# Performance work log

Hardware: AMD Instinct MI355X
Metric: run time of the kernel (lower is better)

## Reference

```python
import jax, jax.numpy as jnp
import numpy as np

H = 256  # hidden_size
I = 18   # input_size
B = 1024 # batch
T = 1024 # seq_len


def setup_inputs() -> dict:
    key = jax.random.key(0)
    ks = jax.random.split(key, 8)
    scale = 1.0 / np.sqrt(H)  # matches torch GRUCell uniform init scale roughly
    s = lambda k, shape: jax.random.normal(k, shape, dtype=jnp.float32) * scale
    return {
        "x": jax.random.normal(ks[0], (B, T, I), dtype=jnp.float32),
        # layer 0 GRUCell params (gate order r, z, n as in torch)
        "W_ih0": s(ks[1], (3 * H, I)),
        "W_hh0": s(ks[2], (3 * H, H)),
        "b_ih0": jnp.zeros((3 * H,), dtype=jnp.float32),
        "b_hh0": jnp.zeros((3 * H,), dtype=jnp.float32),
        # layer 1 GRUCell params
        "W_ih1": s(ks[3], (3 * H, H)),
        "W_hh1": s(ks[4], (3 * H, H)),
        "b_ih1": jnp.zeros((3 * H,), dtype=jnp.float32),
        "b_hh1": jnp.zeros((3 * H,), dtype=jnp.float32),
        "fc_w": s(ks[5], (1, H)),
        "fc_b": jnp.zeros((1,), dtype=jnp.float32),
    }


def _gru_cell(x, h, W_ih, W_hh, b_ih, b_hh):
    # torch.nn.GRUCell math, gate order (r, z, n)
    gi = x @ W_ih.T + b_ih  # (B, 3H)
    gh = h @ W_hh.T + b_hh  # (B, 3H)
    ir, iz, inn = jnp.split(gi, 3, axis=-1)
    hr, hz, hn = jnp.split(gh, 3, axis=-1)
    r = jax.nn.sigmoid(ir + hr)
    z = jax.nn.sigmoid(iz + hz)
    n = jnp.tanh(inn + r * hn)
    return (1.0 - z) * n + z * h


def reference(x, W_ih0, W_hh0, b_ih0, b_hh0, W_ih1, W_hh1, b_ih1, b_hh1, fc_w, fc_b):
    batch = x.shape[0]
    hid = W_hh0.shape[1]
    h_init = (jnp.zeros((batch, hid), dtype=x.dtype),
              jnp.zeros((batch, hid), dtype=x.dtype))
    xs = jnp.swapaxes(x, 0, 1)  # (T, B, I) for scan over time

    def step(carry, xt):
        h0, h1 = carry
        h0 = _gru_cell(xt, h0, W_ih0, W_hh0, b_ih0, b_hh0)
        h1 = _gru_cell(h0, h1, W_ih1, W_hh1, b_ih1, b_hh1)
        return (h0, h1), None

    (h0, h1), _ = jax.lax.scan(step, h_init, xs)
    return h1 @ fc_w.T + fc_b  # (B, 1)
```

## Files before the change

kernel.cpp:

```cpp
#include <hip/hip_runtime.h>

#define B_ 1024
#define T_ 1024
#define I_ 18
#define H_ 256
#define NCHUNK 16
#define NSLICE 16

typedef _Float16 f16;
typedef _Float16 f16x8 __attribute__((ext_vector_type(8)));
typedef float f32x4 __attribute__((ext_vector_type(4)));

#define MFMA16(a, b, c) __builtin_amdgcn_mfma_f32_16x16x32_f16((a), (b), (c), 0, 0, 0)
#define SB() __builtin_amdgcn_sched_barrier(0)

#define WF_FRAGS 75
#define WF_SLICE (WF_FRAGS * 512)
#define WF_TOTAL (NSLICE * WF_SLICE)
#define HB0 WF_TOTAL
#define HB_TOTAL (2 * 2 * NCHUNK * 8 * 4 * 512)
#define PART_B ((HB0 + HB_TOTAL) * 2)
#define FLAG_B (PART_B + 1024 * 16 * 4)
#define NFLAGS (NCHUNK * 4 * 32)
#define IDS_B (FLAG_B + NFLAGS * 4)
#define DEC_B (IDS_B + 256 * 4)
#define F_IH0(g) (g)
#define F_HH0(g, kt) (3 + (g) * 8 + (kt))
#define F_IH1(g, kt) (27 + (g) * 8 + (kt))
#define F_HH1(g, kt) (51 + (g) * 8 + (kt))

struct TrueT { static constexpr bool value = true; };
struct FalseT { static constexpr bool value = false; };

__device__ __forceinline__ int hfrag(int layer, int par, int chunk, int kt, int m) {
  return ((((layer * 2 + par) * NCHUNK + chunk) * 8 + kt) * 4 + m) * 512;
}

__global__ void init_ws(f16* __restrict__ ws) {
  int i = blockIdx.x * blockDim.x + threadIdx.x;
  unsigned* hb = (unsigned*)(ws + HB0);
  for (int k = i; k < HB_TOTAL / 2; k += gridDim.x * blockDim.x) hb[k] = 0u;
  int* flg = (int*)((char*)ws + FLAG_B);
  if (i < NFLAGS + 256 + 1) flg[i] = 0;
}

__global__ void prep_weights(const float* __restrict__ Wih0,
                             const float* __restrict__ Whh0,
                             const float* __restrict__ Wih1,
                             const float* __restrict__ Whh1,
                             f16* __restrict__ ws) {
  int tid = blockIdx.x * blockDim.x + threadIdx.x;
  if (tid >= NSLICE * WF_FRAGS * 64) return;
  int lane = tid & 63;
  int f = (tid >> 6) % WF_FRAGS;
  int s = tid / (WF_FRAGS * 64);
  int lrow = lane & 15, lgrp = lane >> 4;
  f16 v[8];
  if (f < 3) {
    int n = f * H_ + s * 16 + lrow;
#pragma unroll
    for (int j = 0; j < 8; ++j) {
      int k = lgrp * 8 + j;
      v[j] = (k < I_) ? (f16)Wih0[n * I_ + k] : (f16)0.f;
    }
  } else {
    int ff;
    const float* W;
    if (f < 27) { ff = f - 3;  W = Whh0; }
    else if (f < 51) { ff = f - 27; W = Wih1; }
    else { ff = f - 51; W = Whh1; }
    int g = ff >> 3, kt = ff & 7;
    int n = g * H_ + s * 16 + lrow;
    int kb = kt * 32 + lgrp * 8;
#pragma unroll
    for (int j = 0; j < 8; ++j) v[j] = (f16)W[n * H_ + kb + j];
  }
  *(f16x8*)(ws + ((size_t)s * WF_SLICE + f * 512 + lane * 8)) = *(f16x8*)v;
}

__device__ __forceinline__ float sigm(float v) {
  v = fminf(fmaxf(v, -30.f), 30.f);
  return __builtin_amdgcn_rcpf(1.f + __expf(-v));
}
__device__ __forceinline__ float tanh_fast(float v) {
  v = fminf(fmaxf(v, -15.f), 15.f);
  float e = __expf(-2.f * v);
  return (1.f - e) * __builtin_amdgcn_rcpf(1.f + e);
}

template <bool FAST>
__device__ __forceinline__ f16x8 ldh(const f16* p) {
  f16x8 r;
  if (FAST)
    asm volatile("global_load_dwordx4 %0, %1, off nt" : "=&v"(r) : "v"(p));
  else
    asm volatile("global_load_dwordx4 %0, %1, off sc0 sc1" : "=&v"(r) : "v"(p));
  return r;
}
template <bool FAST>
__device__ __forceinline__ void sth(f16* p, f16 v) {
  unsigned u = (unsigned)__builtin_bit_cast(unsigned short, v);
  if (FAST)
    asm volatile("global_store_short %0, %1, off" ::"v"(p), "v"(u) : "memory");
  else
    asm volatile("global_store_short %0, %1, off sc0 sc1" ::"v"(p), "v"(u)
                 : "memory");
}
template <bool FAST>
__device__ __forceinline__ void stf(int* p, int v) {
  if (FAST)
    asm volatile("global_store_dword %0, %1, off" ::"v"(p), "v"(v) : "memory");
  else
    asm volatile("global_store_dword %0, %1, off sc0 sc1" ::"v"(p), "v"(v)
                 : "memory");
}
__device__ __forceinline__ int ld_sys(const int* p) {
  int r;
  asm volatile("global_load_dword %0, %1, off sc0 sc1\n\ts_waitcnt vmcnt(0)"
               : "=&v"(r) : "v"(p) : "memory");
  return r;
}
__device__ __forceinline__ void st_sys(int* p, int v) { stf<false>(p, v); }
__device__ __forceinline__ f32x4 ldx4(const float* p) {
  f32x4 r;
  asm volatile("global_load_dwordx4 %0, %1, off" : "=&v"(r) : "v"(p));
  return r;
}

__global__ __launch_bounds__(256, 1) void gru_main(
    const float* __restrict__ x, const float* __restrict__ bih0,
    const float* __restrict__ bhh0, const float* __restrict__ bih1,
    const float* __restrict__ bhh1, const float* __restrict__ fcw,
    f16* __restrict__ ws) {
  const int tid = threadIdx.x;
  const int wv = tid >> 6, lane = tid & 63;
  const int lrow = lane & 15, lgrp = lane >> 4;
  const int chunk = blockIdx.x & 15, slice = blockIdx.x >> 4;

  f16x8 wf[WF_FRAGS];
  {
    const f16* wb = ws + (size_t)slice * WF_SLICE + lane * 8;
#pragma unroll
    for (int f = 0; f < WF_FRAGS; ++f) wf[f] = *(const f16x8*)(wb + f * 512);
  }

  const int c = slice * 16 + lrow;
  const float bR0 = bih0[c] + bhh0[c], bZ0 = bih0[H_ + c] + bhh0[H_ + c];
  const float bI0 = bih0[2 * H_ + c], bH0 = bhh0[2 * H_ + c];
  const float bR1 = bih1[c] + bhh1[c], bZ1 = bih1[H_ + c] + bhh1[H_ + c];
  const float bI1 = bih1[2 * H_ + c], bH1 = bhh1[2 * H_ + c];
  const float fw = fcw[c];

  float h0r[4] = {0.f, 0.f, 0.f, 0.f}, h1r[4] = {0.f, 0.f, 0.f, 0.f};

  f16* hb = ws + HB0;
  int* flags = (int*)((char*)ws + FLAG_B);
  const int* fpoll = flags + (chunk * 4 + wv) * 32 + (lane & 31);
  int* fpost0 = flags + (chunk * 4 + wv) * 32 + slice;
  int* fpost1 = fpost0 + 16;
  int* ids = (int*)((char*)ws + IDS_B);
  int* dec = (int*)((char*)ws + DEC_B);
  const int rbase = chunk * 64 + wv * 16;
  const float* xrow = x + (size_t)(rbase + lrow) * T_ * I_;
  const int s_kt = slice >> 1;
  const int s_off = 128 * ((slice & 1) * 2 + (lrow >> 3)) + (lrow & 7);
  const int o1 = (lgrp == 0) ? 0 : (lgrp == 1) ? 8 : (lgrp == 2) ? 14 : 0;
  const int o2 = (lgrp == 0) ? 4 : (lgrp == 1) ? 12 : 0;
  int dead = 0;

  {
    unsigned xcc;
    asm volatile("s_getreg_b32 %0, hwreg(HW_REG_XCC_ID)" : "=s"(xcc));
    if (tid == 0) st_sys(ids + blockIdx.x, (int)xcc + 1);
    if (blockIdx.x == 0 && wv == 0) {
      int ok, guard = 0;
      for (;;) {
        int v0 = ld_sys(ids + lane * 4 + 0), v1 = ld_sys(ids + lane * 4 + 1);
        int v2 = ld_sys(ids + lane * 4 + 2), v3 = ld_sys(ids + lane * 4 + 3);
        ok = (v0 && v1 && v2 && v3);
        if (__all(ok)) { ok = 1; break; }
        if (++guard > (1 << 16)) { ok = 0; break; }
        __builtin_amdgcn_s_sleep(8);
      }
      int verdict = 1;
      if (ok) {
        int eq = 1;
        if (lane < 16) {
          int r0 = ld_sys(ids + lane);
          for (int s = 1; s < 16; ++s)
            eq &= (ld_sys(ids + s * 16 + lane) == r0);
        }
        verdict = __all(eq) ? 2 : 1;
      }
      if (lane == 0) st_sys(dec, verdict);
    }
  }
  int decision = 1;
  {
    int g = 0;
    for (;;) {
      int d = ld_sys(dec);
      if (d) { decision = d; break; }
      if (++g > (1 << 20)) break;
      __builtin_amdgcn_s_sleep(8);
    }
  }

  auto phase_loop = [&](auto FC) {
    constexpr bool F = decltype(FC)::value;
    asm volatile("s_waitcnt vmcnt(0)" ::: "memory");
    SB();
    f32x4 xA1 = ldx4(xrow + o1);
    f32x4 xA2 = ldx4(xrow + o2);

    for (int p = 0; p <= T_; ++p) {
      if (p > 0 && !dead) {
        int tgt = (lane & 16) ? p - 1 : p;
        int guard = 0;
        for (;;) {
          int v;
          if (F)
            asm volatile("global_load_dword %0, %1, off nt"
                         : "=&v"(v) : "v"(fpoll));
          else
            asm volatile("global_load_dword %0, %1, off sc0 sc1"
                         : "=&v"(v) : "v"(fpoll));
          asm volatile("s_waitcnt vmcnt(0)" ::: "memory");
          if (__all(v >= tgt)) break;
          if (++guard > (1 << 18)) { dead = 1; break; }
          __builtin_amdgcn_s_sleep(1);
        }
      }
      SB();
      f16x8 ah0[8], ah1[8];
      {
        const f16* b0 = hb + hfrag(0, (p + 1) & 1, chunk, 0, wv) + lane * 8;
        const f16* b1 = hb + hfrag(1, p & 1, chunk, 0, wv) + lane * 8;
#pragma unroll
        for (int kt = 0; kt < 8; ++kt) ah0[kt] = ldh<F>(b0 + kt * 2048);
#pragma unroll
        for (int kt = 0; kt < 8; ++kt) ah1[kt] = ldh<F>(b1 + kt * 2048);
      }
      SB();
      asm volatile("s_waitcnt vmcnt(12)" ::: "memory");
      SB();
      f16x8 ax;
      {
        float s0 = (lgrp == 2) ? xA1[2] : xA1[0];
        float s1 = (lgrp == 2) ? xA1[3] : xA1[1];
        ax[0] = (f16)s0;     ax[1] = (f16)s1;
        ax[2] = (f16)xA1[2]; ax[3] = (f16)xA1[3];
        ax[4] = (f16)xA2[0]; ax[5] = (f16)xA2[1];
        ax[6] = (f16)xA2[2]; ax[7] = (f16)xA2[3];
      }
      f32x4 aR0 = {bR0, bR0, bR0, bR0}, aZ0 = {bZ0, bZ0, bZ0, bZ0};
      f32x4 aI0 = {bI0, bI0, bI0, bI0}, aH0 = {bH0, bH0, bH0, bH0};
      f32x4 aR1 = {bR1, bR1, bR1, bR1}, aZ1 = {bZ1, bZ1, bZ1, bZ1};
      f32x4 aI1 = {bI1, bI1, bI1, bI1}, aH1 = {bH1, bH1, bH1, bH1};
#pragma unroll
      for (int kt = 0; kt < 4; ++kt) {
        aR0 = MFMA16(ah0[kt], wf[F_HH0(0, kt)], aR0);
        aZ0 = MFMA16(ah0[kt], wf[F_HH0(1, kt)], aZ0);
        aH0 = MFMA16(ah0[kt], wf[F_HH0(2, kt)], aH0);
      }
      SB();
      asm volatile("s_waitcnt vmcnt(8)" ::: "memory");
      SB();
      aR0 = MFMA16(ax, wf[F_IH0(0)], aR0);
      aZ0 = MFMA16(ax, wf[F_IH0(1)], aZ0);
      aI0 = MFMA16(ax, wf[F_IH0(2)], aI0);
#pragma unroll
      for (int kt = 4; kt < 8; ++kt) {
        aR0 = MFMA16(ah0[kt], wf[F_HH0(0, kt)], aR0);
        aZ0 = MFMA16(ah0[kt], wf[F_HH0(1, kt)], aZ0);
        aH0 = MFMA16(ah0[kt], wf[F_HH0(2, kt)], aH0);
      }
      if (p < T_) {
        f16* d0 = hb + hfrag(0, p & 1, chunk, s_kt, wv) + s_off;
#pragma unroll
        for (int i = 0; i < 4; ++i) {
          float rr = sigm(aR0[i]);
          float zz = sigm(aZ0[i]);
          float nn = tanh_fast(aI0[i] + rr * aH0[i]);
          h0r[i] = (1.f - zz) * nn + zz * h0r[i];
          sth<F>(d0 + (lgrp * 4 + i) * 8, (f16)h0r[i]);
        }
      }
      SB();
      asm volatile("s_waitcnt vmcnt(0)" ::: "memory");
      SB();
      if (p < T_ && lane == 0) stf<F>(fpost0, p + 1);
#pragma unroll
      for (int kt = 0; kt < 8; ++kt) {
        aR1 = MFMA16(ah0[kt], wf[F_IH1(0, kt)], aR1);
        aZ1 = MFMA16(ah0[kt], wf[F_IH1(1, kt)], aZ1);
        aI1 = MFMA16(ah0[kt], wf[F_IH1(2, kt)], aI1);
        aR1 = MFMA16(ah1[kt], wf[F_HH1(0, kt)], aR1);
        aZ1 = MFMA16(ah1[kt], wf[F_HH1(1, kt)], aZ1);
        aH1 = MFMA16(ah1[kt], wf[F_HH1(2, kt)], aH1);
      }
      if (p > 0) {
        f16* d1 = hb + hfrag(1, (p + 1) & 1, chunk, s_kt, wv) + s_off;
#pragma unroll
        for (int i = 0; i < 4; ++i) {
          float rr = sigm(aR1[i]);
          float zz = sigm(aZ1[i]);
          float nn = tanh_fast(aI1[i] + rr * aH1[i]);
          h1r[i] = (1.f - zz) * nn + zz * h1r[i];
          sth<F>(d1 + (lgrp * 4 + i) * 8, (f16)h1r[i]);
        }
      }
      {
        int tn = (p + 1 < T_) ? p + 1 : T_ - 1;
        const float* px = xrow + (size_t)tn * I_;
        xA1 = ldx4(px + o1);
        xA2 = ldx4(px + o2);
      }
      SB();
      asm volatile("s_waitcnt vmcnt(2)" ::: "memory");
      SB();
      if (p > 0 && lane == 0) stf<F>(fpost1, p);
    }
  };
  if (decision == 2) phase_loop(TrueT{});
  else phase_loop(FalseT{});

  float tmp[4];
#pragma unroll
  for (int i = 0; i < 4; ++i) {
    float v = h1r[i] * fw;
#pragma unroll
    for (int m = 1; m < 16; m <<= 1) v += __shfl_xor(v, m);
    tmp[i] = v;
  }
  if (lrow == 0) {
    float* part = (float*)((char*)ws + PART_B);
#pragma unroll
    for (int i = 0; i < 4; ++i)
      part[(size_t)(rbase + lgrp * 4 + i) * 16 + slice] = tmp[i];
  }
}

__global__ void fc_reduce(const f16* __restrict__ ws,
                          const float* __restrict__ fcb,
                          float* __restrict__ out) {
  int r = blockIdx.x * blockDim.x + threadIdx.x;
  if (r < B_) {
    const float* part = (const float*)((const char*)ws + PART_B);
    float s = fcb[0];
#pragma unroll
    for (int i = 0; i < 16; ++i) s += part[r * 16 + i];
    out[r] = s;
  }
}

extern "C" void kernel_launch(void* const* d_in, const int* in_sizes, int n_in,
                              void* d_out, int out_size, void* d_ws, size_t ws_size,
                              hipStream_t stream) {
  const float* x    = (const float*)d_in[0];
  const float* Wih0 = (const float*)d_in[1];
  const float* Whh0 = (const float*)d_in[2];
  const float* bih0 = (const float*)d_in[3];
  const float* bhh0 = (const float*)d_in[4];
  const float* Wih1 = (const float*)d_in[5];
  const float* Whh1 = (const float*)d_in[6];
  const float* bih1 = (const float*)d_in[7];
  const float* bhh1 = (const float*)d_in[8];
  const float* fcw  = (const float*)d_in[9];
  const float* fcb  = (const float*)d_in[10];

  f16* ws = (f16*)d_ws;

  init_ws<<<1024, 256, 0, stream>>>(ws);
  prep_weights<<<300, 256, 0, stream>>>(Wih0, Whh0, Wih1, Whh1, ws);
  gru_main<<<256, 256, 0, stream>>>(x, bih0, bhh0, bih1, bhh1, fcw, ws);
  fc_reduce<<<4, 256, 0, stream>>>(ws, fcb, (float*)d_out);
}
```

Baseline: 2.096 ms.

## Split GRU layers into separate producer/consumer wavefronts with deeper h0 ring buffer

After: 2.005 ms. 1.05x faster.

```diff
diff --git a/kernel.cpp b/kernel.cpp
--- a/kernel.cpp
+++ b/kernel.cpp
@@ -17,30 +17,20 @@
 #define WF_FRAGS 75
 #define WF_SLICE (WF_FRAGS * 512)
 #define WF_TOTAL (NSLICE * WF_SLICE)
-#define HB0 WF_TOTAL
-#define HB_TOTAL (2 * 2 * NCHUNK * 8 * 4 * 512)
-#define PART_B ((HB0 + HB_TOTAL) * 2)
-#define FLAG_B (PART_B + 1024 * 16 * 4)
+#define H_SLOT (NCHUNK * 8 * 4 * 512)
 #define NFLAGS (NCHUNK * 4 * 32)
-#define IDS_B (FLAG_B + NFLAGS * 4)
-#define DEC_B (IDS_B + 256 * 4)
-#define F_IH0(g) (g)
-#define F_HH0(g, kt) (3 + (g) * 8 + (kt))
-#define F_IH1(g, kt) (27 + (g) * 8 + (kt))
-#define F_HH1(g, kt) (51 + (g) * 8 + (kt))
 
 struct TrueT { static constexpr bool value = true; };
 struct FalseT { static constexpr bool value = false; };
 
-__device__ __forceinline__ int hfrag(int layer, int par, int chunk, int kt, int m) {
-  return ((((layer * 2 + par) * NCHUNK + chunk) * 8 + kt) * 4 + m) * 512;
-}
-
-__global__ void init_ws(f16* __restrict__ ws) {
+__device__ __forceinline__ int hoff(int chunk, int kt, int m) {
+  return (((chunk * 8) + kt) * 4 + m) * 512;
+}
+
+__global__ void init_ws(f16* __restrict__ hb, int hcount, int* __restrict__ flg) {
   int i = blockIdx.x * blockDim.x + threadIdx.x;
-  unsigned* hb = (unsigned*)(ws + HB0);
-  for (int k = i; k < HB_TOTAL / 2; k += gridDim.x * blockDim.x) hb[k] = 0u;
-  int* flg = (int*)((char*)ws + FLAG_B);
+  unsigned* p = (unsigned*)hb;
+  for (int k = i; k < hcount / 2; k += gridDim.x * blockDim.x) p[k] = 0u;
   if (i < NFLAGS + 256 + 1) flg[i] = 0;
 }
 
@@ -79,11 +69,10 @@
 }
 
 __device__ __forceinline__ float sigm(float v) {
-  v = fminf(fmaxf(v, -30.f), 30.f);
   return __builtin_amdgcn_rcpf(1.f + __expf(-v));
 }
 __device__ __forceinline__ float tanh_fast(float v) {
-  v = fminf(fmaxf(v, -15.f), 15.f);
+  v = fmaxf(v, -15.f);
   float e = __expf(-2.f * v);
   return (1.f - e) * __builtin_amdgcn_rcpf(1.f + e);
 }
@@ -127,46 +116,31 @@
   return r;
 }
 
-__global__ __launch_bounds__(256, 1) void gru_main(
+__global__ __launch_bounds__(512, 2) void gru_main(
     const float* __restrict__ x, const float* __restrict__ bih0,
     const float* __restrict__ bhh0, const float* __restrict__ bih1,
     const float* __restrict__ bhh1, const float* __restrict__ fcw,
-    f16* __restrict__ ws) {
+    const f16* __restrict__ wfr, f16* __restrict__ hb0, f16* __restrict__ hb1,
+    float* __restrict__ part, int* __restrict__ flags, int* __restrict__ ids,
+    int* __restrict__ dec, int hmask) {
+  __shared__ f16 whh1_l[24 * 512];
+
   const int tid = threadIdx.x;
   const int wv = tid >> 6, lane = tid & 63;
+  const int w = wv & 3;
+  const bool isL0 = wv < 4;
   const int lrow = lane & 15, lgrp = lane >> 4;
   const int chunk = blockIdx.x & 15, slice = blockIdx.x >> 4;
 
-  f16x8 wf[WF_FRAGS];
-  {
-    const f16* wb = ws + (size_t)slice * WF_SLICE + lane * 8;
-#pragma unroll
-    for (int f = 0; f < WF_FRAGS; ++f) wf[f] = *(const f16x8*)(wb + f * 512);
-  }
+  for (int i = tid; i < 24 * 64; i += 512)
+    ((f16x8*)whh1_l)[i] =
+        ((const f16x8*)(wfr + (size_t)slice * WF_SLICE + 51 * 512))[i];
 
   const int c = slice * 16 + lrow;
-  const float bR0 = bih0[c] + bhh0[c], bZ0 = bih0[H_ + c] + bhh0[H_ + c];
-  const float bI0 = bih0[2 * H_ + c], bH0 = bhh0[2 * H_ + c];
-  const float bR1 = bih1[c] + bhh1[c], bZ1 = bih1[H_ + c] + bhh1[H_ + c];
-  const float bI1 = bih1[2 * H_ + c], bH1 = bhh1[2 * H_ + c];
-  const float fw = fcw[c];
-
-  float h0r[4] = {0.f, 0.f, 0.f, 0.f}, h1r[4] = {0.f, 0.f, 0.f, 0.f};
-
-  f16* hb = ws + HB0;
-  int* flags = (int*)((char*)ws + FLAG_B);
-  const int* fpoll = flags + (chunk * 4 + wv) * 32 + (lane & 31);
-  int* fpost0 = flags + (chunk * 4 + wv) * 32 + slice;
-  int* fpost1 = fpost0 + 16;
-  int* ids = (int*)((char*)ws + IDS_B);
-  int* dec = (int*)((char*)ws + DEC_B);
-  const int rbase = chunk * 64 + wv * 16;
-  const float* xrow = x + (size_t)(rbase + lrow) * T_ * I_;
+  const int* fpoll = flags + (chunk * 4 + w) * 32 + (lane & 31);
+  const int rbase = chunk * 64 + w * 16;
   const int s_kt = slice >> 1;
   const int s_off = 128 * ((slice & 1) * 2 + (lrow >> 3)) + (lrow & 7);
-  const int o1 = (lgrp == 0) ? 0 : (lgrp == 1) ? 8 : (lgrp == 2) ? 14 : 0;
-  const int o2 = (lgrp == 0) ? 4 : (lgrp == 1) ? 12 : 0;
-  int dead = 0;
 
   {
     unsigned xcc;
@@ -205,148 +179,225 @@
       __builtin_amdgcn_s_sleep(8);
     }
   }
-
-  auto phase_loop = [&](auto FC) {
-    constexpr bool F = decltype(FC)::value;
-    asm volatile("s_waitcnt vmcnt(0)" ::: "memory");
-    SB();
-    f32x4 xA1 = ldx4(xrow + o1);
-    f32x4 xA2 = ldx4(xrow + o2);
-
-    for (int p = 0; p <= T_; ++p) {
-      if (p > 0 && !dead) {
-        int tgt = (lane & 16) ? p - 1 : p;
-        int guard = 0;
-        for (;;) {
-          int v;
-          if (F)
-            asm volatile("global_load_dword %0, %1, off nt"
-                         : "=&v"(v) : "v"(fpoll));
-          else
-            asm volatile("global_load_dword %0, %1, off sc0 sc1"
-                         : "=&v"(v) : "v"(fpoll));
-          asm volatile("s_waitcnt vmcnt(0)" ::: "memory");
-          if (__all(v >= tgt)) break;
-          if (++guard > (1 << 18)) { dead = 1; break; }
-          __builtin_amdgcn_s_sleep(1);
-        }
-      }
-      SB();
-      f16x8 ah0[8], ah1[8];
-      {
-        const f16* b0 = hb + hfrag(0, (p + 1) & 1, chunk, 0, wv) + lane * 8;
-        const f16* b1 = hb + hfrag(1, p & 1, chunk, 0, wv) + lane * 8;
-#pragma unroll
-        for (int kt = 0; kt < 8; ++kt) ah0[kt] = ldh<F>(b0 + kt * 2048);
-#pragma unroll
-        for (int kt = 0; kt < 8; ++kt) ah1[kt] = ldh<F>(b1 + kt * 2048);
-      }
-      SB();
-      asm volatile("s_waitcnt vmcnt(12)" ::: "memory");
-      SB();
-      f16x8 ax;
-      {
-        float s0 = (lgrp == 2) ? xA1[2] : xA1[0];
-        float s1 = (lgrp == 2) ? xA1[3] : xA1[1];
-        ax[0] = (f16)s0;     ax[1] = (f16)s1;
-        ax[2] = (f16)xA1[2]; ax[3] = (f16)xA1[3];
-        ax[4] = (f16)xA2[0]; ax[5] = (f16)xA2[1];
-        ax[6] = (f16)xA2[2]; ax[7] = (f16)xA2[3];
-      }
-      f32x4 aR0 = {bR0, bR0, bR0, bR0}, aZ0 = {bZ0, bZ0, bZ0, bZ0};
-      f32x4 aI0 = {bI0, bI0, bI0, bI0}, aH0 = {bH0, bH0, bH0, bH0};
-      f32x4 aR1 = {bR1, bR1, bR1, bR1}, aZ1 = {bZ1, bZ1, bZ1, bZ1};
-      f32x4 aI1 = {bI1, bI1, bI1, bI1}, aH1 = {bH1, bH1, bH1, bH1};
-#pragma unroll
-      for (int kt = 0; kt < 4; ++kt) {
-        aR0 = MFMA16(ah0[kt], wf[F_HH0(0, kt)], aR0);
-        aZ0 = MFMA16(ah0[kt], wf[F_HH0(1, kt)], aZ0);
-        aH0 = MFMA16(ah0[kt], wf[F_HH0(2, kt)], aH0);
-      }
-      SB();
-      asm volatile("s_waitcnt vmcnt(8)" ::: "memory");
-      SB();
-      aR0 = MFMA16(ax, wf[F_IH0(0)], aR0);
-      aZ0 = MFMA16(ax, wf[F_IH0(1)], aZ0);
-      aI0 = MFMA16(ax, wf[F_IH0(2)], aI0);
-#pragma unroll
-      for (int kt = 4; kt < 8; ++kt) {
-        aR0 = MFMA16(ah0[kt], wf[F_HH0(0, kt)], aR0);
-        aZ0 = MFMA16(ah0[kt], wf[F_HH0(1, kt)], aZ0);
-        aH0 = MFMA16(ah0[kt], wf[F_HH0(2, kt)], aH0);
-      }
-      if (p < T_) {
-        f16* d0 = hb + hfrag(0, p & 1, chunk, s_kt, wv) + s_off;
-#pragma unroll
-        for (int i = 0; i < 4; ++i) {
-          float rr = sigm(aR0[i]);
-          float zz = sigm(aZ0[i]);
-          float nn = tanh_fast(aI0[i] + rr * aH0[i]);
-          h0r[i] = (1.f - zz) * nn + zz * h0r[i];
-          sth<F>(d0 + (lgrp * 4 + i) * 8, (f16)h0r[i]);
-        }
-      }
-      SB();
+  __syncthreads();
+
+  if (isL0) {
+    f16x8 wfA[27];
+    {
+      const f16* wb = wfr + (size_t)slice * WF_SLICE + lane * 8;
+#pragma unroll
+      for (int f = 0; f < 27; ++f) wfA[f] = *(const f16x8*)(wb + f * 512);
+    }
+    const float bR0 = bih0[c] + bhh0[c], bZ0 = bih0[H_ + c] + bhh0[H_ + c];
+    const float bI0 = bih0[2 * H_ + c], bH0 = bhh0[2 * H_ + c];
+    float h0r[4] = {0.f, 0.f, 0.f, 0.f};
+    int* fpost0 = flags + (chunk * 4 + w) * 32 + slice;
+    const float* xrow = x + (size_t)(rbase + lrow) * T_ * I_;
+    const int o1 = (lgrp == 0) ? 0 : (lgrp == 1) ? 8 : (lgrp == 2) ? 14 : 0;
+    const int o2 = (lgrp == 0) ? 4 : (lgrp == 1) ? 12 : 0;
+    int dead = 0;
+
+    auto loop0 = [&](auto FC) {
+      constexpr bool F = decltype(FC)::value;
       asm volatile("s_waitcnt vmcnt(0)" ::: "memory");
       SB();
-      if (p < T_ && lane == 0) stf<F>(fpost0, p + 1);
-#pragma unroll
-      for (int kt = 0; kt < 8; ++kt) {
-        aR1 = MFMA16(ah0[kt], wf[F_IH1(0, kt)], aR1);
-        aZ1 = MFMA16(ah0[kt], wf[F_IH1(1, kt)], aZ1);
-        aI1 = MFMA16(ah0[kt], wf[F_IH1(2, kt)], aI1);
-        aR1 = MFMA16(ah1[kt], wf[F_HH1(0, kt)], aR1);
-        aZ1 = MFMA16(ah1[kt], wf[F_HH1(1, kt)], aZ1);
-        aH1 = MFMA16(ah1[kt], wf[F_HH1(2, kt)], aH1);
+      f32x4 xA1 = ldx4(xrow + o1);
+      f32x4 xA2 = ldx4(xrow + o2);
+      for (int p = 0; p < T_; ++p) {
+        if (p > 0 && !dead) {
+          int tgt = (lane & 16) ? (p - hmask) : p;
+          int guard = 0;
+          for (;;) {
+            int v;
+            if (F)
+              asm volatile("global_load_dword %0, %1, off nt"
+                           : "=&v"(v) : "v"(fpoll));
+            else
+              asm volatile("global_load_dword %0, %1, off sc0 sc1"
+                           : "=&v"(v) : "v"(fpoll));
+            asm volatile("s_waitcnt vmcnt(0)" ::: "memory");
+            if (__all(v >= tgt)) break;
+            if (++guard > (1 << 18)) { dead = 1; break; }
+          }
+        }
+        SB();
+        __builtin_amdgcn_s_setprio(1);
+        f16x8 ah0[8];
+        {
+          const f16* b0 = hb0 + (size_t)((p - 1) & hmask) * H_SLOT +
+                          hoff(chunk, 0, w) + lane * 8;
+#pragma unroll
+          for (int kt = 0; kt < 8; ++kt) ah0[kt] = ldh<F>(b0 + kt * 2048);
+        }
+        SB();
+        asm volatile("s_waitcnt vmcnt(4)" ::: "memory");
+        SB();
+        f16x8 ax;
+        {
+          float s0 = (lgrp == 2) ? xA1[2] : xA1[0];
+          float s1 = (lgrp == 2) ? xA1[3] : xA1[1];
+          ax[0] = (f16)s0;     ax[1] = (f16)s1;
+          ax[2] = (f16)xA1[2]; ax[3] = (f16)xA1[3];
+          ax[4] = (f16)xA2[0]; ax[5] = (f16)xA2[1];
+          ax[6] = (f16)xA2[2]; ax[7] = (f16)xA2[3];
+        }
+        f32x4 aR = {bR0, bR0, bR0, bR0}, aZ = {bZ0, bZ0, bZ0, bZ0};
+        f32x4 aI = {bI0, bI0, bI0, bI0}, aH = {bH0, bH0, bH0, bH0};
+        aR = MFMA16(ax, wfA[0], aR);
+        aZ = MFMA16(ax, wfA[1], aZ);
+        aI = MFMA16(ax, wfA[2], aI);
+#pragma unroll
+        for (int kt = 0; kt < 4; ++kt) {
+          aR = MFMA16(ah0[kt], wfA[3 + kt], aR);
+          aZ = MFMA16(ah0[kt], wfA[11 + kt], aZ);
+          aH = MFMA16(ah0[kt], wfA[19 + kt], aH);
+        }
+        SB();
+        asm volatile("s_waitcnt vmcnt(0)" ::: "memory");
+        SB();
+#pragma unroll
+        for (int kt = 4; kt < 8; ++kt) {
+          aR = MFMA16(ah0[kt], wfA[3 + kt], aR);
+          aZ = MFMA16(ah0[kt], wfA[11 + kt], aZ);
+          aH = MFMA16(ah0[kt], wfA[19 + kt], aH);
+        }
+        {
+          f16* d0 = hb0 + (size_t)(p & hmask) * H_SLOT +
+                    hoff(chunk, s_kt, w) + s_off;
+#pragma unroll
+          for (int i = 0; i < 4; ++i) {
+            float rr = sigm(aR[i]);
+            float zz = sigm(aZ[i]);
+            float nn = tanh_fast(aI[i] + rr * aH[i]);
+            h0r[i] = (1.f - zz) * nn + zz * h0r[i];
+            sth<F>(d0 + (lgrp * 4 + i) * 8, (f16)h0r[i]);
+          }
+        }
+        SB();
+        asm volatile("s_waitcnt vmcnt(0)" ::: "memory");
+        SB();
+        if (lane == 0) stf<F>(fpost0, p + 1);
+        __builtin_amdgcn_s_setprio(0);
+        {
+          int tn = (p + 1 < T_) ? p + 1 : T_ - 1;
+          const float* px = xrow + (size_t)tn * I_;
+          xA1 = ldx4(px + o1);
+          xA2 = ldx4(px + o2);
+        }
       }
-      if (p > 0) {
-        f16* d1 = hb + hfrag(1, (p + 1) & 1, chunk, s_kt, wv) + s_off;
-#pragma unroll
-        for (int i = 0; i < 4; ++i) {
-          float rr = sigm(aR1[i]);
-          float zz = sigm(aZ1[i]);
-          float nn = tanh_fast(aI1[i] + rr * aH1[i]);
-          h1r[i] = (1.f - zz) * nn + zz * h1r[i];
-          sth<F>(d1 + (lgrp * 4 + i) * 8, (f16)h1r[i]);
-        }
+    };
+    if (decision == 2) loop0(TrueT{});
+    else loop0(FalseT{});
+  } else {
+    f16x8 wfB[24];
+    {
+      const f16* wb = wfr + (size_t)slice * WF_SLICE + 27 * 512 + lane * 8;
+#pragma unroll
+      for (int f = 0; f < 24; ++f) wfB[f] = *(const f16x8*)(wb + f * 512);
+    }
+    const float bR1 = bih1[c] + bhh1[c], bZ1 = bih1[H_ + c] + bhh1[H_ + c];
+    const float bI1 = bih1[2 * H_ + c], bH1 = bhh1[2 * H_ + c];
+    const float fw = fcw[c];
+    float h1r[4] = {0.f, 0.f, 0.f, 0.f};
+    int* fpost1 = flags + (chunk * 4 + w) * 32 + 16 + slice;
+    int dead = 0;
+
+    auto loop1 = [&](auto FC) {
+      constexpr bool F = decltype(FC)::value;
+      for (int p = 1; p <= T_; ++p) {
+        if (!dead) {
+          int tgt = (lane & 16) ? (p - 1) : p;
+          int guard = 0;
+          for (;;) {
+            int v;
+            if (F)
+              asm volatile("global_load_dword %0, %1, off nt"
+                           : "=&v"(v) : "v"(fpoll));
+            else
+              asm volatile("global_load_dword %0, %1, off sc0 sc1"
+                           : "=&v"(v) : "v"(fpoll));
+            asm volatile("s_waitcnt vmcnt(0)" ::: "memory");
+            if (__all(v >= tgt)) break;
+            if (++guard > (1 << 18)) { dead = 1; break; }
+          }
+        }
+        SB();
+        f16x8 ah0[8], ah1[8];
+        {
+          const f16* b0 = hb0 + (size_t)((p - 1) & hmask) * H_SLOT +
+                          hoff(chunk, 0, w) + lane * 8;
+          const f16* b1 = hb1 + (size_t)(p & 1) * H_SLOT +
+                          hoff(chunk, 0, w) + lane * 8;
+#pragma unroll
+          for (int kt = 0; kt < 8; ++kt) ah0[kt] = ldh<F>(b0 + kt * 2048);
+#pragma unroll
+          for (int kt = 0; kt < 8; ++kt) ah1[kt] = ldh<F>(b1 + kt * 2048);
+        }
+        SB();
+        asm volatile("s_waitcnt vmcnt(8)" ::: "memory");
+        SB();
+        f32x4 aR = {bR1, bR1, bR1, bR1}, aZ = {bZ1, bZ1, bZ1, bZ1};
+        f32x4 aI = {bI1, bI1, bI1, bI1}, aH = {bH1, bH1, bH1, bH1};
+#pragma unroll
+        for (int kt = 0; kt < 8; ++kt) {
+          aR = MFMA16(ah0[kt], wfB[kt], aR);
+          aZ = MFMA16(ah0[kt], wfB[8 + kt], aZ);
+          aI = MFMA16(ah0[kt], wfB[16 + kt], aI);
+        }
+        SB();
+        asm volatile("s_waitcnt vmcnt(0)" ::: "memory");
+        SB();
+#pragma unroll
+        for (int kt = 0; kt < 8; ++kt) {
+          f16x8 br = *(const f16x8*)&whh1_l[(0 * 8 + kt) * 512 + lane * 8];
+          f16x8 bz = *(const f16x8*)&whh1_l[(1 * 8 + kt) * 512 + lane * 8];
+          f16x8 bn = *(const f16x8*)&whh1_l[(2 * 8 + kt) * 512 + lane * 8];
+          aR = MFMA16(ah1[kt], br, aR);
+          aZ = MFMA16(ah1[kt], bz, aZ);
+          aH = MFMA16(ah1[kt], bn, aH);
+        }
+        {
+          f16* d1 = hb1 + (size_t)((p - 1) & 1) * H_SLOT +
+                    hoff(chunk, s_kt, w) + s_off;
+#pragma unroll
+          for (int i = 0; i < 4; ++i) {
+            float rr = sigm(aR[i]);
+            float zz = sigm(aZ[i]);
+            float nn = tanh_fast(aI[i] + rr * aH[i]);
+            h1r[i] = (1.f - zz) * nn + zz * h1r[i];
+            sth<F>(d1 + (lgrp * 4 + i) * 8, (f16)h1r[i]);
+          }
+        }
+        SB();
+        asm volatile("s_waitcnt vmcnt(0)" ::: "memory");
+        SB();
+        if (lane == 0) stf<F>(fpost1, p);
       }
-      {
-        int tn = (p + 1 < T_) ? p + 1 : T_ - 1;
-        const float* px = xrow + (size_t)tn * I_;
-        xA1 = ldx4(px + o1);
-        xA2 = ldx4(px + o2);
-      }
-      SB();
-      asm volatile("s_waitcnt vmcnt(2)" ::: "memory");
-      SB();
-      if (p > 0 && lane == 0) stf<F>(fpost1, p);
-    }
-  };
-  if (decision == 2) phase_loop(TrueT{});
-  else phase_loop(FalseT{});
-
-  float tmp[4];
-#pragma unroll
-  for (int i = 0; i < 4; ++i) {
-    float v = h1r[i] * fw;
-#pragma unroll
-    for (int m = 1; m < 16; m <<= 1) v += __shfl_xor(v, m);
-    tmp[i] = v;
+    };
+    if (decision == 2) loop1(TrueT{});
+    else loop1(FalseT{});
+
+    float tmp[4];
+#pragma unroll
+    for (int i = 0; i < 4; ++i) {
+      float v = h1r[i] * fw;
+#pragma unroll
+      for (int m = 1; m < 16; m <<= 1) v += __shfl_xor(v, m);
+      tmp[i] = v;
+    }
+    if (lrow == 0) {
+#pragma unroll
+      for (int i = 0; i < 4; ++i)
+        part[(size_t)(rbase + lgrp * 4 + i) * 16 + slice] = tmp[i];
+    }
   }
-  if (lrow == 0) {
-    float* part = (float*)((char*)ws + PART_B);
-#pragma unroll
-    for (int i = 0; i < 4; ++i)
-      part[(size_t)(rbase + lgrp * 4 + i) * 16 + slice] = tmp[i];
-  }
-}
-
-__global__ void fc_reduce(const f16* __restrict__ ws,
+}
+
+__global__ void fc_reduce(const float* __restrict__ part,
                           const float* __restrict__ fcb,
                           float* __restrict__ out) {
   int r = blockIdx.x * blockDim.x + threadIdx.x;
   if (r < B_) {
-    const float* part = (const float*)((const char*)ws + PART_B);
     float s = fcb[0];
 #pragma unroll
     for (int i = 0; i < 16; ++i) s += part[r * 16 + i];
@@ -369,10 +420,21 @@
   const float* fcw  = (const float*)d_in[9];
   const float* fcb  = (const float*)d_in[10];
 
-  f16* ws = (f16*)d_ws;
-
-  init_ws<<<1024, 256, 0, stream>>>(ws);
-  prep_weights<<<300, 256, 0, stream>>>(Wih0, Whh0, Wih1, Whh1, ws);
-  gru_main<<<256, 256, 0, stream>>>(x, bih0, bhh0, bih1, bhh1, fcw, ws);
-  fc_reduce<<<4, 256, 0, stream>>>(ws, fcb, (float*)d_out);
-}
+  size_t tail = 1024 * 16 * 4 + (NFLAGS + 256 + 8) * 4;
+  size_t need4 = (size_t)(WF_TOTAL + 6 * H_SLOT) * 2 + tail;
+  int hmask = (ws_size >= need4) ? 3 : 1;
+  f16* wfr = (f16*)d_ws;
+  f16* hb0 = wfr + WF_TOTAL;
+  f16* hb1 = hb0 + (size_t)(hmask + 1) * H_SLOT;
+  float* part = (float*)(hb1 + 2 * H_SLOT);
+  int* flags = (int*)(part + 1024 * 16);
+  int* ids = flags + NFLAGS;
+  int* dec = ids + 256;
+  int hcount = (hmask + 3) * H_SLOT;
+
+  init_ws<<<1024, 256, 0, stream>>>(hb0, hcount, flags);
+  prep_weights<<<300, 256, 0, stream>>>(Wih0, Whh0, Wih1, Whh1, wfr);
+  gru_main<<<256, 512, 0, stream>>>(x, bih0, bhh0, bih1, bhh1, fcw, wfr, hb0,
+                                    hb1, part, flags, ids, dec, hmask);
+  fc_reduce<<<4, 256, 0, stream>>>(part, fcb, (float*)d_out);
+}
```
